# Kernel optimization log

Measured on AMD Instinct MI355X. Metric: run time of the kernel, lower is better.

## Reference

```python
import jax, jax.numpy as jnp
import numpy as np

DIM = 512
NUM_HEADS = 8
HEAD_DIM = DIM // NUM_HEADS
SCALE = HEAD_DIM ** -0.5


def setup_inputs() -> dict:
    key = jax.random.key(0)
    ks = jax.random.split(key, 10)
    B, Sq, Skv = 4, 2048, 2048
    std = DIM ** -0.5
    return {
        "x1": jax.random.normal(ks[0], (B, Sq, DIM), jnp.float32),
        "x2": jax.random.normal(ks[1], (B, Skv, DIM), jnp.float32),
        "Wq": jax.random.normal(ks[2], (DIM, DIM), jnp.float32) * std,
        "bq": jax.random.normal(ks[3], (DIM,), jnp.float32) * 0.02,
        "Wk": jax.random.normal(ks[4], (DIM, DIM), jnp.float32) * std,
        "bk": jax.random.normal(ks[5], (DIM,), jnp.float32) * 0.02,
        "Wv": jax.random.normal(ks[6], (DIM, DIM), jnp.float32) * std,
        "bv": jax.random.normal(ks[7], (DIM,), jnp.float32) * 0.02,
        "Wo": jax.random.normal(ks[8], (DIM, DIM), jnp.float32) * std,
        "bo": jax.random.normal(ks[9], (DIM,), jnp.float32) * 0.02,
    }


def reference(x1, x2, Wq, bq, Wk, bk, Wv, bv, Wo, bo):
    B, Sq, _ = x1.shape
    Skv = x2.shape[1]
    # Linear projections (torch nn.Linear: x @ W.T + b)
    Q = (x1 @ Wq.T + bq).reshape(B, Sq, NUM_HEADS, HEAD_DIM)
    K = (x2 @ Wk.T + bk).reshape(B, Skv, NUM_HEADS, HEAD_DIM)
    V = (x2 @ Wv.T + bv).reshape(B, Skv, NUM_HEADS, HEAD_DIM)
    # [B, H, Sq, Skv]
    attn = jnp.einsum("bqhd,bkhd->bhqk", Q, K) * SCALE
    attn = jax.nn.softmax(attn, axis=-1)  # dropout is identity in eval mode
    out = jnp.einsum("bhqk,bkhd->bqhd", attn, V).reshape(B, Sq, DIM)
    return out @ Wo.T + bo
```

## Files before the change

### kernel.cpp

```cpp
#include <hip/hip_runtime.h>
#include <math.h>

constexpr int kB = 4, kS = 2048, kDim = 512, kNH = 8, kHD = 64;
constexpr float kQScale = 0.18033688011112042f;

using bf16x8 = __attribute__((ext_vector_type(8))) short;
using f32x4  = __attribute__((ext_vector_type(4))) float;

__device__ __forceinline__ unsigned pack_rn(float f0, float f1) {
  unsigned a = __builtin_bit_cast(unsigned, f0) + 0x8000u;
  unsigned b = __builtin_bit_cast(unsigned, f1) + 0x8000u;
  return __builtin_amdgcn_perm(b, a, 0x07060302u);
}
__device__ __forceinline__ float fexp2(float x) {
#if __has_builtin(__builtin_amdgcn_exp2f)
  return __builtin_amdgcn_exp2f(x);
#else
  return exp2f(x);
#endif
}

#define GLDS(gp, lp) __builtin_amdgcn_global_load_lds(                         \
    (const __attribute__((address_space(1))) void*)(gp),                       \
    (__attribute__((address_space(3))) void*)(lp), 16, 0, 0)

__global__ __launch_bounds__(256) void cvt_bf16(
    const float* __restrict__ x1, const float* __restrict__ x2,
    const float* __restrict__ Wq, const float* __restrict__ Wk,
    const float* __restrict__ Wv, const float* __restrict__ Wo,
    unsigned short* __restrict__ x1b, unsigned short* __restrict__ x2b,
    unsigned short* __restrict__ wb) {
  const size_t i = (size_t)blockIdx.x * 256 + threadIdx.x;
  const float* src;
  unsigned short* dst;
  size_t off;
  if (i < 1048576) { src = x1; dst = x1b; off = i; }
  else if (i < 2097152) { src = x2; dst = x2b; off = i - 1048576; }
  else {
    const size_t j = i - 2097152;
    const int seg = (int)(j >> 16);
    src = seg == 0 ? Wq : seg == 1 ? Wk : seg == 2 ? Wv : Wo;
    dst = wb + (size_t)seg * 262144;
    off = j & 65535;
  }
  const float4 v = *(const float4*)(src + off * 4);
  uint2 o;
  o.x = pack_rn(v.x, v.y);
  o.y = pack_rn(v.z, v.w);
  *(uint2*)(dst + off * 4) = o;
}

__global__ __launch_bounds__(256, 2) void qkv_gemm(
    const unsigned short* __restrict__ x1b, const unsigned short* __restrict__ x2b,
    const unsigned short* __restrict__ wb,
    const float* __restrict__ bq, const float* __restrict__ bk,
    const float* __restrict__ bv,
    unsigned short* __restrict__ Qg, unsigned short* __restrict__ Kg,
    unsigned short* __restrict__ Vg) {
  __shared__ __align__(16) short As[2][128 * 64];
  __shared__ __align__(16) short Bs[2][128 * 64];
  const int z = blockIdx.z;
  const unsigned short* X = z ? x2b : x1b;
  const unsigned short* W = wb + (size_t)z * (kDim * kDim);
  const float* bias = (z == 0) ? bq : (z == 1) ? bk : bv;

  const int t = threadIdx.x, lane = t & 63, w = t >> 6;
  const int g = lane >> 4, c = lane & 15;
  const int bm = blockIdx.y * 128, bn = blockIdx.x * 128;
  const int wm = (w >> 1) * 64, wn = (w & 1) * 64;

  const int srow = lane >> 3;
  const int schunk = ((lane & 7) ^ srow) * 8;
  const int wrow = w * 32;

#pragma unroll
  for (int i8 = 0; i8 < 4; ++i8) {
    const int row = wrow + i8 * 8;
    GLDS(X + (size_t)(bm + row + srow) * kDim + schunk, &As[0][row * 64]);
    GLDS(W + (size_t)(bn + row + srow) * kDim + schunk, &Bs[0][row * 64]);
  }
  __syncthreads();

  f32x4 acc[16] = {};
  int ib = 0;
  for (int k0 = 0; k0 < kDim; k0 += 64, ib ^= 1) {
    if (k0 + 64 < kDim) {
      const int nb = ib ^ 1;
#pragma unroll
      for (int i8 = 0; i8 < 4; ++i8) {
        const int row = wrow + i8 * 8;
        GLDS(X + (size_t)(bm + row + srow) * kDim + k0 + 64 + schunk, &As[nb][row * 64]);
        GLDS(W + (size_t)(bn + row + srow) * kDim + k0 + 64 + schunk, &Bs[nb][row * 64]);
      }
    }
#pragma unroll
    for (int kk = 0; kk < 2; ++kk) {
      const int sx = ((kk * 4 + g) ^ (c & 7)) * 8;
      if (z == 2) {
        bf16x8 fa[4], fb[4];
#pragma unroll
        for (int i = 0; i < 4; ++i) fa[i] = *(const bf16x8*)&As[ib][(wm + i * 16 + c) * 64 + sx];
#pragma unroll
        for (int j = 0; j < 4; ++j) fb[j] = *(const bf16x8*)&Bs[ib][(wn + j * 16 + c) * 64 + sx];
#pragma unroll
        for (int i = 0; i < 4; ++i)
#pragma unroll
          for (int j = 0; j < 4; ++j)
            acc[i * 4 + j] = __builtin_amdgcn_mfma_f32_16x16x32_bf16(fa[i], fb[j], acc[i * 4 + j], 0, 0, 0);
      } else {
        bf16x8 fa[4], fb[4];
#pragma unroll
        for (int i = 0; i < 4; ++i) fa[i] = *(const bf16x8*)&Bs[ib][(wn + i * 16 + c) * 64 + sx];
#pragma unroll
        for (int j = 0; j < 4; ++j) fb[j] = *(const bf16x8*)&As[ib][(wm + j * 16 + c) * 64 + sx];
#pragma unroll
        for (int i = 0; i < 4; ++i)
#pragma unroll
          for (int j = 0; j < 4; ++j)
            acc[i * 4 + j] = __builtin_amdgcn_mfma_f32_16x16x32_bf16(fa[i], fb[j], acc[i * 4 + j], 0, 0, 0);
      }
    }
    __syncthreads();
  }

  if (z == 2) {
    const int h_ = (bn + wn) >> 6;
#pragma unroll
    for (int i = 0; i < 4; ++i)
#pragma unroll
      for (int j = 0; j < 4; ++j) {
        const int n = bn + wn + j * 16 + c;
        const float bb = bias[n];
        const int m0 = bm + wm + i * 16 + g * 4;
        const int b_ = m0 >> 11, s0 = m0 & 2047;
        const int d_ = n & 63;
        const f32x4 a = acc[i * 4 + j];
        uint2 pv;
        pv.x = pack_rn(a[0] + bb, a[1] + bb);
        pv.y = pack_rn(a[2] + bb, a[3] + bb);
        *(uint2*)(Vg + (((size_t)((b_ * kNH + h_) * kHD + d_)) << 11) + s0) = pv;
      }
  } else {
    const float sc = (z == 0) ? kQScale : 1.0f;
    unsigned short* Og = z ? Kg : Qg;
    const int h_ = (bn + wn) >> 6;
#pragma unroll
    for (int i = 0; i < 4; ++i) {
      const int n0 = bn + wn + i * 16 + g * 4;
      const float4 bb = *(const float4*)(bias + n0);
      const int d0 = n0 & 63;
#pragma unroll
      for (int j = 0; j < 4; ++j) {
        const int m = bm + wm + j * 16 + c;
        const int b_ = m >> 11, s_ = m & 2047;
        const f32x4 a = acc[i * 4 + j];
        uint2 st;
        st.x = pack_rn((a[0] + bb.x) * sc, (a[1] + bb.y) * sc);
        st.y = pack_rn((a[2] + bb.z) * sc, (a[3] + bb.w) * sc);
        *(uint2*)(Og + (((size_t)((b_ * kNH + h_) * kS + s_)) << 6) + d0) = st;
      }
    }
  }
}

__global__ __launch_bounds__(256, 2) void out_gemm(const unsigned short* __restrict__ A,
                                                   const unsigned short* __restrict__ Wob,
                                                   const float* __restrict__ bias,
                                                   float* __restrict__ Y) {
  __shared__ __align__(16) short As[2][128 * 64];
  __shared__ __align__(16) short Bs[2][128 * 64];
  const int t = threadIdx.x, lane = t & 63, w = t >> 6;
  const int g = lane >> 4, c = lane & 15;
  const int bm = blockIdx.y * 128, bn = blockIdx.x * 128;
  const int wm = (w >> 1) * 64, wn = (w & 1) * 64;
  const int srow = lane >> 3;
  const int schunk = ((lane & 7) ^ srow) * 8;
  const int wrow = w * 32;

#pragma unroll
  for (int i8 = 0; i8 < 4; ++i8) {
    const int row = wrow + i8 * 8;
    GLDS(A + (size_t)(bm + row + srow) * kDim + schunk, &As[0][row * 64]);
    GLDS(Wob + (size_t)(bn + row + srow) * kDim + schunk, &Bs[0][row * 64]);
  }
  __syncthreads();

  f32x4 acc[16] = {};
  int ib = 0;
  for (int k0 = 0; k0 < kDim; k0 += 64, ib ^= 1) {
    if (k0 + 64 < kDim) {
      const int nb = ib ^ 1;
#pragma unroll
      for (int i8 = 0; i8 < 4; ++i8) {
        const int row = wrow + i8 * 8;
        GLDS(A + (size_t)(bm + row + srow) * kDim + k0 + 64 + schunk, &As[nb][row * 64]);
        GLDS(Wob + (size_t)(bn + row + srow) * kDim + k0 + 64 + schunk, &Bs[nb][row * 64]);
      }
    }
#pragma unroll
    for (int kk = 0; kk < 2; ++kk) {
      const int sx = ((kk * 4 + g) ^ (c & 7)) * 8;
      bf16x8 fa[4], fb[4];
#pragma unroll
      for (int i = 0; i < 4; ++i) fa[i] = *(const bf16x8*)&Bs[ib][(wn + i * 16 + c) * 64 + sx];
#pragma unroll
      for (int j = 0; j < 4; ++j) fb[j] = *(const bf16x8*)&As[ib][(wm + j * 16 + c) * 64 + sx];
#pragma unroll
      for (int i = 0; i < 4; ++i)
#pragma unroll
        for (int j = 0; j < 4; ++j)
          acc[i * 4 + j] = __builtin_amdgcn_mfma_f32_16x16x32_bf16(fa[i], fb[j], acc[i * 4 + j], 0, 0, 0);
    }
    __syncthreads();
  }
#pragma unroll
  for (int i = 0; i < 4; ++i) {
    const int n0 = bn + wn + i * 16 + g * 4;
    const float4 bb = *(const float4*)(bias + n0);
#pragma unroll
    for (int j = 0; j < 4; ++j) {
      const int m = bm + wm + j * 16 + c;
      const f32x4 a = acc[i * 4 + j];
      float4 st;
      st.x = a[0] + bb.x;
      st.y = a[1] + bb.y;
      st.z = a[2] + bb.z;
      st.w = a[3] + bb.w;
      *(float4*)(Y + (size_t)m * kDim + n0) = st;
    }
  }
}

__global__ __launch_bounds__(256, 2) void flash_mfma(const unsigned short* __restrict__ Qg,
                                                     const unsigned short* __restrict__ Kg,
                                                     const unsigned short* __restrict__ Vg,
                                                     unsigned short* __restrict__ attn) {
  __shared__ __align__(16) short Ks[64 * 76];
  __shared__ __align__(16) short Vs[64 * 76];
  const int t = threadIdx.x, lane = t & 63, w = t >> 6;
  const int c = lane & 15, g4 = lane >> 4;
  const int bh = blockIdx.x, q0 = blockIdx.y * 128;
  const int b_ = bh >> 3, h_ = bh & 7;

  const unsigned short* Qp = Qg + ((size_t)bh * kS + q0) * kHD;
  const unsigned short* Kp = Kg + (size_t)bh * kS * kHD;
  const unsigned short* Vp = Vg + (size_t)bh * kHD * kS;

  bf16x8 bq[2][2];
  {
    const unsigned short* qr = Qp + (size_t)(w * 32 + c) * kHD + g4 * 8;
    bq[0][0] = *(const bf16x8*)qr;
    bq[1][0] = *(const bf16x8*)(qr + 32);
    bq[0][1] = *(const bf16x8*)(qr + 16 * kHD);
    bq[1][1] = *(const bf16x8*)(qr + 16 * kHD + 32);
  }

  const int r0 = t >> 3, cc0 = (t & 7) * 8;
  const int ps = (((r0 >> 2) & 1) << 4) | (((r0 >> 3) & 3) << 2) | (r0 & 3);
  const unsigned short* kpt = Kp + (size_t)r0 * kHD + cc0;
  const unsigned short* vpt = Vp + (size_t)r0 * kS + cc0;
  uint4 pk0 = *(const uint4*)kpt;
  uint4 pk1 = *(const uint4*)(kpt + 32 * kHD);
  uint4 pv0 = *(const uint4*)vpt;
  uint4 pv1 = *(const uint4*)(vpt + 32 * kS);
  kpt += 64 * kHD;
  vpt += 64;

  float l[2] = {0.f, 0.f};
  f32x4 o[4][2] = {};

  for (int kv0 = 0; kv0 < kS; kv0 += 64) {
    __syncthreads();
    *(uint4*)&Ks[ps * 76 + cc0] = pk0;
    *(uint4*)&Ks[(ps + 32) * 76 + cc0] = pk1;
    *(uint4*)&Vs[r0 * 76 + cc0] = pv0;
    *(uint4*)&Vs[(r0 + 32) * 76 + cc0] = pv1;
    __syncthreads();
    if (kv0 + 64 < kS) {
      pk0 = *(const uint4*)kpt;
      pk1 = *(const uint4*)(kpt + 32 * kHD);
      pv0 = *(const uint4*)vpt;
      pv1 = *(const uint4*)(vpt + 32 * kS);
      kpt += 64 * kHD;
      vpt += 64;
    }

    f32x4 sa[4][2] = {};
#pragma unroll
    for (int ks = 0; ks < 2; ++ks)
#pragma unroll
      for (int kt = 0; kt < 4; ++kt) {
        const bf16x8 a = *(const bf16x8*)&Ks[(kt * 16 + c) * 76 + ks * 32 + g4 * 8];
        sa[kt][0] = __builtin_amdgcn_mfma_f32_16x16x32_bf16(a, bq[ks][0], sa[kt][0], 0, 0, 0);
        sa[kt][1] = __builtin_amdgcn_mfma_f32_16x16x32_bf16(a, bq[ks][1], sa[kt][1], 0, 0, 0);
      }

#pragma unroll
    for (int ks = 0; ks < 2; ++ks) {
      bf16x8 bpf[2];
#pragma unroll
      for (int qs = 0; qs < 2; ++qs) {
        const float p0 = fexp2(sa[2 * ks][qs][0]), p1 = fexp2(sa[2 * ks][qs][1]);
        const float p2 = fexp2(sa[2 * ks][qs][2]), p3 = fexp2(sa[2 * ks][qs][3]);
        const float p4 = fexp2(sa[2 * ks + 1][qs][0]), p5 = fexp2(sa[2 * ks + 1][qs][1]);
        const float p6 = fexp2(sa[2 * ks + 1][qs][2]), p7 = fexp2(sa[2 * ks + 1][qs][3]);
        l[qs] += ((p0 + p1) + (p2 + p3)) + ((p4 + p5) + (p6 + p7));
        uint4 bp;
        bp.x = pack_rn(p0, p1);
        bp.y = pack_rn(p2, p3);
        bp.z = pack_rn(p4, p5);
        bp.w = pack_rn(p6, p7);
        bpf[qs] = __builtin_bit_cast(bf16x8, bp);
      }
#pragma unroll
      for (int dt = 0; dt < 4; ++dt) {
        const bf16x8 va = *(const bf16x8*)&Vs[(dt * 16 + c) * 76 + ks * 32 + g4 * 8];
        o[dt][0] = __builtin_amdgcn_mfma_f32_16x16x32_bf16(va, bpf[0], o[dt][0], 0, 0, 0);
        o[dt][1] = __builtin_amdgcn_mfma_f32_16x16x32_bf16(va, bpf[1], o[dt][1], 0, 0, 0);
      }
    }
  }

#pragma unroll
  for (int qs = 0; qs < 2; ++qs) {
    l[qs] += __shfl_xor(l[qs], 16, 64);
    l[qs] += __shfl_xor(l[qs], 32, 64);
  }
#pragma unroll
  for (int qs = 0; qs < 2; ++qs) {
    const float inv = 1.0f / l[qs];
    unsigned short* orow =
        attn + ((size_t)(b_ * kS + q0 + w * 32 + qs * 16 + c)) * kDim + h_ * kHD;
#pragma unroll
    for (int dt = 0; dt < 4; ++dt) {
      uint2 st;
      st.x = pack_rn(o[dt][qs][0] * inv, o[dt][qs][1] * inv);
      st.y = pack_rn(o[dt][qs][2] * inv, o[dt][qs][3] * inv);
      *(uint2*)(orow + dt * 16 + g4 * 4) = st;
    }
  }
}

extern "C" void kernel_launch(void* const* d_in, const int* in_sizes, int n_in,
                              void* d_out, int out_size, void* d_ws, size_t ws_size,
                              hipStream_t stream) {
  const float* x1 = (const float*)d_in[0];
  const float* x2 = (const float*)d_in[1];
  const float* Wq = (const float*)d_in[2];
  const float* bq = (const float*)d_in[3];
  const float* Wk = (const float*)d_in[4];
  const float* bk = (const float*)d_in[5];
  const float* Wv = (const float*)d_in[6];
  const float* bv = (const float*)d_in[7];
  const float* Wo = (const float*)d_in[8];
  const float* bo = (const float*)d_in[9];
  float* out = (float*)d_out;

  constexpr size_t kTok = (size_t)kB * kS * kDim;
  unsigned short* x1b = (unsigned short*)d_ws;
  unsigned short* x2b = x1b + kTok;
  unsigned short* wb  = x2b + kTok;
  unsigned short* Qg  = wb + 4 * (size_t)(kDim * kDim);
  unsigned short* Kg  = Qg + kTok;
  unsigned short* Vg  = Kg + kTok;
  unsigned short* atb = Vg + kTok;

  const dim3 blk(256);
  cvt_bf16<<<dim3(9216), blk, 0, stream>>>(x1, x2, Wq, Wk, Wv, Wo, x1b, x2b, wb);
  qkv_gemm<<<dim3(4, 64, 3), blk, 0, stream>>>(x1b, x2b, wb, bq, bk, bv, Qg, Kg, Vg);
  flash_mfma<<<dim3(32, 16), blk, 0, stream>>>(Qg, Kg, Vg, atb);
  out_gemm<<<dim3(4, 64), blk, 0, stream>>>(atb, wb + 3 * (size_t)(kDim * kDim), bo, out);
}
```

Before: 178.6 us.

## Fuse activation bf16 conversion into QKV GEMM tile loads

Removes the separate fp32-to-bf16 conversion pass for x1/x2; the QKV GEMM now loads fp32 activations into registers, packs them to bf16, and writes swizzled tiles to LDS during compute. The standalone convert kernel now only converts weights. This avoids writing and re-reading bf16 activation copies, at the cost of register-staged loads instead of direct global-to-LDS loads, doubled load bytes per tile, and dropping the min-blocks launch bound.

Measured after the change: 187.3 us. 1.05x slower.

```diff
diff --git a/kernel.cpp b/kernel.cpp
--- a/kernel.cpp
+++ b/kernel.cpp
@@ -24,25 +24,15 @@
     (const __attribute__((address_space(1))) void*)(gp),                       \
     (__attribute__((address_space(3))) void*)(lp), 16, 0, 0)
 
-__global__ __launch_bounds__(256) void cvt_bf16(
-    const float* __restrict__ x1, const float* __restrict__ x2,
+__global__ __launch_bounds__(256) void cvt_w(
     const float* __restrict__ Wq, const float* __restrict__ Wk,
     const float* __restrict__ Wv, const float* __restrict__ Wo,
-    unsigned short* __restrict__ x1b, unsigned short* __restrict__ x2b,
     unsigned short* __restrict__ wb) {
   const size_t i = (size_t)blockIdx.x * 256 + threadIdx.x;
-  const float* src;
-  unsigned short* dst;
-  size_t off;
-  if (i < 1048576) { src = x1; dst = x1b; off = i; }
-  else if (i < 2097152) { src = x2; dst = x2b; off = i - 1048576; }
-  else {
-    const size_t j = i - 2097152;
-    const int seg = (int)(j >> 16);
-    src = seg == 0 ? Wq : seg == 1 ? Wk : seg == 2 ? Wv : Wo;
-    dst = wb + (size_t)seg * 262144;
-    off = j & 65535;
-  }
+  const int seg = (int)(i >> 16);
+  const size_t off = i & 65535;
+  const float* src = seg == 0 ? Wq : seg == 1 ? Wk : seg == 2 ? Wv : Wo;
+  unsigned short* dst = wb + (size_t)seg * 262144;
   const float4 v = *(const float4*)(src + off * 4);
   uint2 o;
   o.x = pack_rn(v.x, v.y);
@@ -50,8 +40,8 @@
   *(uint2*)(dst + off * 4) = o;
 }
 
-__global__ __launch_bounds__(256, 2) void qkv_gemm(
-    const unsigned short* __restrict__ x1b, const unsigned short* __restrict__ x2b,
+__global__ __launch_bounds__(256) void qkv_gemm(
+    const float* __restrict__ x1, const float* __restrict__ x2,
     const unsigned short* __restrict__ wb,
     const float* __restrict__ bq, const float* __restrict__ bk,
     const float* __restrict__ bv,
@@ -60,7 +50,7 @@
   __shared__ __align__(16) short As[2][128 * 64];
   __shared__ __align__(16) short Bs[2][128 * 64];
   const int z = blockIdx.z;
-  const unsigned short* X = z ? x2b : x1b;
+  const float* X = z ? x2 : x1;
   const unsigned short* W = wb + (size_t)z * (kDim * kDim);
   const float* bias = (z == 0) ? bq : (z == 1) ? bk : bv;
 
@@ -73,23 +63,55 @@
   const int schunk = ((lane & 7) ^ srow) * 8;
   const int wrow = w * 32;
 
-#pragma unroll
-  for (int i8 = 0; i8 < 4; ++i8) {
-    const int row = wrow + i8 * 8;
-    GLDS(X + (size_t)(bm + row + srow) * kDim + schunk, &As[0][row * 64]);
-    GLDS(W + (size_t)(bn + row + srow) * kDim + schunk, &Bs[0][row * 64]);
+  const int arow = t >> 2;
+  const int acf = (t & 3) * 16;
+
+  {
+    float4 v[2][4];
+#pragma unroll
+    for (int rep = 0; rep < 2; ++rep) {
+      const float* src = X + (size_t)(bm + rep * 64 + arow) * kDim + acf;
+#pragma unroll
+      for (int i = 0; i < 4; ++i) v[rep][i] = ((const float4*)src)[i];
+    }
+#pragma unroll
+    for (int rep = 0; rep < 2; ++rep) {
+      const int row = rep * 64 + arow;
+#pragma unroll
+      for (int ch = 0; ch < 2; ++ch) {
+        const float4 a0 = v[rep][ch * 2], a1 = v[rep][ch * 2 + 1];
+        uint4 u;
+        u.x = pack_rn(a0.x, a0.y);
+        u.y = pack_rn(a0.z, a0.w);
+        u.z = pack_rn(a1.x, a1.y);
+        u.w = pack_rn(a1.z, a1.w);
+        const int lch = (t & 3) * 2 + ch;
+        *(uint4*)&As[0][row * 64 + (lch ^ (row & 7)) * 8] = u;
+      }
+    }
+#pragma unroll
+    for (int i8 = 0; i8 < 4; ++i8) {
+      const int row = wrow + i8 * 8;
+      GLDS(W + (size_t)(bn + row + srow) * kDim + schunk, &Bs[0][row * 64]);
+    }
   }
   __syncthreads();
 
   f32x4 acc[16] = {};
   int ib = 0;
   for (int k0 = 0; k0 < kDim; k0 += 64, ib ^= 1) {
+    const int nb = ib ^ 1;
+    float4 v[2][4];
     if (k0 + 64 < kDim) {
-      const int nb = ib ^ 1;
+#pragma unroll
+      for (int rep = 0; rep < 2; ++rep) {
+        const float* src = X + (size_t)(bm + rep * 64 + arow) * kDim + k0 + 64 + acf;
+#pragma unroll
+        for (int i = 0; i < 4; ++i) v[rep][i] = ((const float4*)src)[i];
+      }
 #pragma unroll
       for (int i8 = 0; i8 < 4; ++i8) {
         const int row = wrow + i8 * 8;
-        GLDS(X + (size_t)(bm + row + srow) * kDim + k0 + 64 + schunk, &As[nb][row * 64]);
         GLDS(W + (size_t)(bn + row + srow) * kDim + k0 + 64 + schunk, &Bs[nb][row * 64]);
       }
     }
@@ -118,6 +140,23 @@
 #pragma unroll
           for (int j = 0; j < 4; ++j)
             acc[i * 4 + j] = __builtin_amdgcn_mfma_f32_16x16x32_bf16(fa[i], fb[j], acc[i * 4 + j], 0, 0, 0);
+      }
+    }
+    if (k0 + 64 < kDim) {
+#pragma unroll
+      for (int rep = 0; rep < 2; ++rep) {
+        const int row = rep * 64 + arow;
+#pragma unroll
+        for (int ch = 0; ch < 2; ++ch) {
+          const float4 a0 = v[rep][ch * 2], a1 = v[rep][ch * 2 + 1];
+          uint4 u;
+          u.x = pack_rn(a0.x, a0.y);
+          u.y = pack_rn(a0.z, a0.w);
+          u.z = pack_rn(a1.x, a1.y);
+          u.w = pack_rn(a1.z, a1.w);
+          const int lch = (t & 3) * 2 + ch;
+          *(uint4*)&As[nb][row * 64 + (lch ^ (row & 7)) * 8] = u;
+        }
       }
     }
     __syncthreads();
@@ -357,17 +396,15 @@
   float* out = (float*)d_out;
 
   constexpr size_t kTok = (size_t)kB * kS * kDim;
-  unsigned short* x1b = (unsigned short*)d_ws;
-  unsigned short* x2b = x1b + kTok;
-  unsigned short* wb  = x2b + kTok;
+  unsigned short* wb  = (unsigned short*)d_ws;
   unsigned short* Qg  = wb + 4 * (size_t)(kDim * kDim);
   unsigned short* Kg  = Qg + kTok;
   unsigned short* Vg  = Kg + kTok;
   unsigned short* atb = Vg + kTok;
 
   const dim3 blk(256);
-  cvt_bf16<<<dim3(9216), blk, 0, stream>>>(x1, x2, Wq, Wk, Wv, Wo, x1b, x2b, wb);
-  qkv_gemm<<<dim3(4, 64, 3), blk, 0, stream>>>(x1b, x2b, wb, bq, bk, bv, Qg, Kg, Vg);
+  cvt_w<<<dim3(1024), blk, 0, stream>>>(Wq, Wk, Wv, Wo, wb);
+  qkv_gemm<<<dim3(4, 64, 3), blk, 0, stream>>>(x1, x2, wb, bq, bk, bv, Qg, Kg, Vg);
   flash_mfma<<<dim3(32, 16), blk, 0, stream>>>(Qg, Kg, Vg, atb);
   out_gemm<<<dim3(4, 64), blk, 0, stream>>>(atb, wb + 3 * (size_t)(kDim * kDim), bo, out);
 }
```
